# Kernel tuning notes

Measured on AMD Instinct MI355X. Metric: run time of the kernel, lower is better.

Reference implementation:

```python
import jax, jax.numpy as jnp
import numpy as np

C = 32          # in_channels = out_channels = groups
K = 3           # kernel_size
STRIDE = 2
PAD = 1
DIL = 1
EPS = 1e-20


def _depthwise_convT(x, w):
    """Equivalent of torch.F.conv_transpose2d(x, w, groups=C, stride=STRIDE,
    padding=PAD, dilation=DIL) with w of shape (C, 1, K, K).
    Implemented as an lhs-dilated conv with a spatially flipped kernel."""
    w_f = w[:, :, ::-1, ::-1]
    pad = DIL * (K - 1) - PAD  # = 1 for K=3, PAD=1, DIL=1
    return jax.lax.conv_general_dilated(
        x, w_f,
        window_strides=(1, 1),
        padding=[(pad, pad), (pad, pad)],
        lhs_dilation=(STRIDE, STRIDE),
        rhs_dilation=(DIL, DIL),
        dimension_numbers=('NCHW', 'OIHW', 'NCHW'),
        feature_group_count=C)


def setup_inputs() -> dict:
    key = jax.random.key(0)
    k = jax.random.split(key, 7)
    B, H, W = 2, 176, 608
    # depths/confidences are positive (rand); gy is signed (randn)
    d = jax.random.uniform(k[0], (B, C, H, W), dtype=jnp.float32) + 0.5
    cd = jax.random.uniform(k[1], (B, C, H, W), dtype=jnp.float32)
    gy = jax.random.normal(k[2], (B, C, H, W), dtype=jnp.float32)
    cgy = jax.random.uniform(k[3], (B, C, H, W), dtype=jnp.float32)
    w_prop_raw = jax.random.normal(k[4], (1, C, 1, 1), dtype=jnp.float32)
    spatial_weight_raw = jax.random.normal(k[5], (C, 1, K, K), dtype=jnp.float32)
    bias = 0.01 * jax.random.normal(k[6], (1, C, 1, 1), dtype=jnp.float32)
    return {"d": d, "cd": cd, "gy": gy, "cgy": cgy,
            "w_prop_raw": w_prop_raw,
            "spatial_weight_raw": spatial_weight_raw,
            "bias": bias}


def reference(d, cd, gy, cgy, w_prop_raw, spatial_weight_raw, bias):
    # EnforcePos('softplus') on both learned weights
    w_prop = jax.nn.softplus(w_prop_raw)          # (1, C, 1, 1)
    sw = jax.nn.softplus(spatial_weight_raw)      # (C, 1, K, K)

    # roll-based vertical neighbor gather with edge confidence zeroing
    d_up = jnp.roll(d, 1, axis=2)
    cd_up = jnp.roll(cd, 1, axis=2).at[:, :, 0, :].set(0.0)
    d_down = jnp.roll(d, -1, axis=2)
    cd_down = jnp.roll(cd, -1, axis=2).at[:, :, -1, :].set(0.0)

    cgy_from_ds = cd_up * cd_up
    height = (cd_up * d_up + cd_down * d_down) / (cd_up + cd_down)
    gy_from_ds = (d_down - d_up) / 2.0 / height

    gy_f = (w_prop * cgy * gy + cgy_from_ds * gy_from_ds) / (w_prop * cgy + cgy_from_ds)
    cgy_f = (w_prop * cgy + cgy_from_ds) / (w_prop + 1.0)

    nom = _depthwise_convT(cgy_f * gy_f, sw)
    denom = _depthwise_convT(cgy_f, sw)
    cdenom = _depthwise_convT(jnp.ones_like(cgy_f), sw)

    # original adds bias twice: once unconditionally, once under use_bias
    gy_out = nom / (denom + EPS) + bias + bias
    cgy_out = denom / (cdenom + EPS)
    return gy_out / STRIDE, cgy_out
```

## Files before the change

kernel.cpp:

```cpp
#include <hip/hip_runtime.h>
#include <math.h>

#define B_   2
#define C_   32
#define H_   176
#define W_   608
#define HO_  351
#define WO_  1215
#define PLANE_O (HO_ * WO_)
#define OUT1_O  (B_ * C_ * PLANE_O)
#define EPS_ 1e-20f
#define NTH  512
#define W4   (W_ / 4)
#define HW_  304

typedef float f4_t __attribute__((ext_vector_type(4)));
typedef float f2_t __attribute__((ext_vector_type(2)));

__device__ __forceinline__ float softplus_f(float x) {
    return fmaxf(x, 0.0f) + log1pf(expf(-fabsf(x)));
}

extern "C" __global__ __launch_bounds__(NTH, 8)
void structn_rows(const float* __restrict__ d,
                  const float* __restrict__ cd,
                  const float* __restrict__ gy,
                  const float* __restrict__ cgy,
                  const float* __restrict__ wpr,
                  const float* __restrict__ swr,
                  const float* __restrict__ bias,
                  float* __restrict__ out)
{
    __shared__ float s_nE[5 * HW_];
    __shared__ float s_nO[5 * HW_];
    __shared__ float s_cE[5 * HW_];
    __shared__ float s_cO[5 * HW_];

    const int g     = blockIdx.x;
    const int plane = blockIdx.y;
    const int c     = plane & (C_ - 1);

    float sw[9];
#pragma unroll
    for (int k = 0; k < 9; ++k) sw[k] = softplus_f(swr[c * 9 + k]);
    const float wp      = softplus_f(wpr[c]);
    const float inv_wp1 = 1.0f / (wp + 1.0f);
    const float bv      = bias[c];
    const float icd_ee  = 1.0f / (sw[4] + EPS_);
    const float icd_eo  = 1.0f / (sw[3] + sw[5] + EPS_);
    const float icd_oe  = 1.0f / (sw[1] + sw[7] + EPS_);
    const float icd_oo  = 1.0f / (sw[0] + sw[2] + sw[6] + sw[8] + EPS_);

    const int r0  = g * 4;
    const int nrf = (r0 + 4 <= H_ - 1) ? 5 : (H_ - r0);

    const int pbase = plane * (H_ * W_);
    const float* __restrict__ dP  = d   + pbase;
    const float* __restrict__ cdP = cd  + pbase;
    const float* __restrict__ gyP = gy  + pbase;
    const float* __restrict__ cgP = cgy + pbase;

    const int ntask = nrf * W4;
    for (int idx = threadIdx.x; idx < ntask; idx += NTH) {
        const int rf = idx / W4;
        const int iw = (idx - rf * W4) << 2;
        const int iy = r0 + rf;
        const int up = (iy == 0)      ? (H_ - 1) : iy - 1;
        const int dn = (iy == H_ - 1) ? 0        : iy + 1;
        const float mu = (iy > 0)      ? 1.0f : 0.0f;
        const float md = (iy < H_ - 1) ? 1.0f : 0.0f;

        const f4_t du = *(const f4_t*)(dP  + up * W_ + iw);
        const f4_t dd = *(const f4_t*)(dP  + dn * W_ + iw);
        const f4_t cu = *(const f4_t*)(cdP + up * W_ + iw);
        const f4_t cn = *(const f4_t*)(cdP + dn * W_ + iw);
        const f4_t gg = *(const f4_t*)(gyP + iy * W_ + iw);
        const f4_t cg = *(const f4_t*)(cgP + iy * W_ + iw);

        f4_t sn4, sc4;
#pragma unroll
        for (int e = 0; e < 4; ++e) {
            const float cuv = cu[e] * mu;
            const float cnv = cn[e] * md;
            const float cfd = cuv * cuv;
            const float rs  = __builtin_amdgcn_rcpf(fmaf(cuv, du[e], cnv * dd[e]));
            const float gfd = 0.5f * (dd[e] - du[e]) * (cuv + cnv) * rs;
            const float num = fmaf(wp * cg[e], gg[e], cfd * gfd);
            const float den = fmaf(wp, cg[e], cfd);
            sn4[e] = num * inv_wp1;
            sc4[e] = den * inv_wp1;
        }
        const int eo = rf * HW_ + (iw >> 1);
        f2_t v;
        v[0] = sn4[0]; v[1] = sn4[2];  *(f2_t*)(s_nE + eo) = v;
        v[0] = sn4[1]; v[1] = sn4[3];  *(f2_t*)(s_nO + eo) = v;
        v[0] = sc4[0]; v[1] = sc4[2];  *(f2_t*)(s_cE + eo) = v;
        v[0] = sc4[1]; v[1] = sc4[3];  *(f2_t*)(s_cO + eo) = v;
    }
    __syncthreads();

    const int w    = threadIdx.x >> 6;
    const int lane = threadIdx.x & 63;
    const int oy   = g * 8 + w;
    if (oy >= HO_) return;

    const int p   = w & 1;
    const int lrA = w >> 1;

    const int ro0 = plane * PLANE_O + oy * WO_;
    float* __restrict__ o0 = out + ro0;
    float* __restrict__ o1 = out + OUT1_O + ro0;

    const int h  = (4 - (ro0 & 3)) & 3;
    const int n4 = (WO_ - h) >> 2;
    const int q  = h & 1;
    const int r  = (h >> 1) & 1;

    const float icdC = p ? icd_oe : icd_ee;
    const float icdO = p ? icd_oo : icd_eo;
    const float i0 = q ? icdO : icdC;
    const float i1 = q ? icdC : icdO;

    const float* __restrict__ nAE = s_nE + lrA * HW_;
    const float* __restrict__ nAO = s_nO + lrA * HW_;
    const float* __restrict__ cAE = s_cE + lrA * HW_;
    const float* __restrict__ cAO = s_cO + lrA * HW_;

#define VAL(E, O, j) (((j) & 1) ? (O)[((j) - 1) >> 1] : (E)[(j) >> 1])

    if (p == 0) {
        if (lane < 3) {
            const int ox = (lane < h) ? lane : (h + (n4 << 2) + lane - h);
            float den, nom, icd;
            if ((ox & 1) == 0) {
                const int j = ox >> 1;
                den = VAL(cAE, cAO, j) * sw[4];
                nom = VAL(nAE, nAO, j) * sw[4];
                icd = icd_ee;
            } else {
                const int j = (ox - 1) >> 1;
                den = VAL(cAE, cAO, j) * sw[5] + VAL(cAE, cAO, j + 1) * sw[3];
                nom = VAL(nAE, nAO, j) * sw[5] + VAL(nAE, nAO, j + 1) * sw[3];
                icd = icd_eo;
            }
            o0[ox] = fmaf(0.5f * nom, __builtin_amdgcn_rcpf(den + EPS_), bv);
            o1[ox] = den * icd;
        }
        const float* pa0 = r ? nAO : nAE;
        const float* pa1 = r ? nAE + 1 : nAO;
        const float* pa2 = r ? nAO + 1 : nAE + 1;
        const float* px0 = r ? cAO : cAE;
        const float* px1 = r ? cAE + 1 : cAO;
        const float* px2 = r ? cAO + 1 : cAE + 1;

        for (int k = lane; k < n4; k += 64) {
            const float a0 = pa0[k], a1 = pa1[k], a2 = pa2[k];
            const float x0 = px0[k], x1 = px1[k], x2 = px2[k];
            const float dC0 = x0 * sw[4], dC1 = x1 * sw[4], dC2 = x2 * sw[4];
            const float nC0 = a0 * sw[4], nC1 = a1 * sw[4], nC2 = a2 * sw[4];
            const float dF0 = x0 * sw[5] + x1 * sw[3];
            const float dF1 = x1 * sw[5] + x2 * sw[3];
            const float nF0 = a0 * sw[5] + a1 * sw[3];
            const float nF1 = a1 * sw[5] + a2 * sw[3];

            const float d0 = q ? dF0 : dC0, n0 = q ? nF0 : nC0;
            const float d1 = q ? dC1 : dF0, n1 = q ? nC1 : nF0;
            const float d2 = q ? dF1 : dC1, n2 = q ? nF1 : nC1;
            const float d3 = q ? dC2 : dF1, n3 = q ? nC2 : nF1;

            f4_t gv, qv;
            gv[0] = fmaf(0.5f * n0, __builtin_amdgcn_rcpf(d0 + EPS_), bv);
            gv[1] = fmaf(0.5f * n1, __builtin_amdgcn_rcpf(d1 + EPS_), bv);
            gv[2] = fmaf(0.5f * n2, __builtin_amdgcn_rcpf(d2 + EPS_), bv);
            gv[3] = fmaf(0.5f * n3, __builtin_amdgcn_rcpf(d3 + EPS_), bv);
            qv[0] = d0 * i0; qv[1] = d1 * i1; qv[2] = d2 * i0; qv[3] = d3 * i1;

            const int c0 = h + (k << 2);
            __builtin_nontemporal_store(gv, (f4_t*)(o0 + c0));
            __builtin_nontemporal_store(qv, (f4_t*)(o1 + c0));
        }
    } else {
        const float* __restrict__ nBE = nAE + HW_;
        const float* __restrict__ nBO = nAO + HW_;
        const float* __restrict__ cBE = cAE + HW_;
        const float* __restrict__ cBO = cAO + HW_;

        if (lane < 3) {
            const int ox = (lane < h) ? lane : (h + (n4 << 2) + lane - h);
            float den, nom, icd;
            if ((ox & 1) == 0) {
                const int j = ox >> 1;
                den = VAL(cAE, cAO, j) * sw[7] + VAL(cBE, cBO, j) * sw[1];
                nom = VAL(nAE, nAO, j) * sw[7] + VAL(nBE, nBO, j) * sw[1];
                icd = icd_oe;
            } else {
                const int j = (ox - 1) >> 1;
                den = VAL(cAE, cAO, j) * sw[8] + VAL(cAE, cAO, j + 1) * sw[6]
                    + VAL(cBE, cBO, j) * sw[2] + VAL(cBE, cBO, j + 1) * sw[0];
                nom = VAL(nAE, nAO, j) * sw[8] + VAL(nAE, nAO, j + 1) * sw[6]
                    + VAL(nBE, nBO, j) * sw[2] + VAL(nBE, nBO, j + 1) * sw[0];
                icd = icd_oo;
            }
            o0[ox] = fmaf(0.5f * nom, __builtin_amdgcn_rcpf(den + EPS_), bv);
            o1[ox] = den * icd;
        }

        const float* pa0 = r ? nAO : nAE;
        const float* pa1 = r ? nAE + 1 : nAO;
        const float* pa2 = r ? nAO + 1 : nAE + 1;
        const float* px0 = r ? cAO : cAE;
        const float* px1 = r ? cAE + 1 : cAO;
        const float* px2 = r ? cAO + 1 : cAE + 1;
        const float* pb0 = r ? nBO : nBE;
        const float* pb1 = r ? nBE + 1 : nBO;
        const float* pb2 = r ? nBO + 1 : nBE + 1;
        const float* py0 = r ? cBO : cBE;
        const float* py1 = r ? cBE + 1 : cBO;
        const float* py2 = r ? cBO + 1 : cBE + 1;

        for (int k = lane; k < n4; k += 64) {
            const float a0 = pa0[k], a1 = pa1[k], a2 = pa2[k];
            const float x0 = px0[k], x1 = px1[k], x2 = px2[k];
            const float b0 = pb0[k], b1 = pb1[k], b2 = pb2[k];
            const float y0 = py0[k], y1 = py1[k], y2 = py2[k];

            const float dC0 = x0 * sw[7] + y0 * sw[1];
            const float dC1 = x1 * sw[7] + y1 * sw[1];
            const float dC2 = x2 * sw[7] + y2 * sw[1];
            const float nC0 = a0 * sw[7] + b0 * sw[1];
            const float nC1 = a1 * sw[7] + b1 * sw[1];
            const float nC2 = a2 * sw[7] + b2 * sw[1];
            const float dF0 = x0 * sw[8] + x1 * sw[6] + y0 * sw[2] + y1 * sw[0];
            const float dF1 = x1 * sw[8] + x2 * sw[6] + y1 * sw[2] + y2 * sw[0];
            const float nF0 = a0 * sw[8] + a1 * sw[6] + b0 * sw[2] + b1 * sw[0];
            const float nF1 = a1 * sw[8] + a2 * sw[6] + b1 * sw[2] + b2 * sw[0];

            const float d0 = q ? dF0 : dC0, n0 = q ? nF0 : nC0;
            const float d1 = q ? dC1 : dF0, n1 = q ? nC1 : nF0;
            const float d2 = q ? dF1 : dC1, n2 = q ? nF1 : nC1;
            const float d3 = q ? dC2 : dF1, n3 = q ? nC2 : nF1;

            f4_t gv, qv;
            gv[0] = fmaf(0.5f * n0, __builtin_amdgcn_rcpf(d0 + EPS_), bv);
            gv[1] = fmaf(0.5f * n1, __builtin_amdgcn_rcpf(d1 + EPS_), bv);
            gv[2] = fmaf(0.5f * n2, __builtin_amdgcn_rcpf(d2 + EPS_), bv);
            gv[3] = fmaf(0.5f * n3, __builtin_amdgcn_rcpf(d3 + EPS_), bv);
            qv[0] = d0 * i0; qv[1] = d1 * i1; qv[2] = d2 * i0; qv[3] = d3 * i1;

            const int c0 = h + (k << 2);
            __builtin_nontemporal_store(gv, (f4_t*)(o0 + c0));
            __builtin_nontemporal_store(qv, (f4_t*)(o1 + c0));
        }
    }
#undef VAL
}

extern "C" void kernel_launch(void* const* d_in, const int* in_sizes, int n_in,
                              void* d_out, int out_size, void* d_ws, size_t ws_size,
                              hipStream_t stream) {
    const float* d    = (const float*)d_in[0];
    const float* cd   = (const float*)d_in[1];
    const float* gy   = (const float*)d_in[2];
    const float* cgy  = (const float*)d_in[3];
    const float* wpr  = (const float*)d_in[4];
    const float* swr  = (const float*)d_in[5];
    const float* bias = (const float*)d_in[6];
    float* out = (float*)d_out;

    dim3 grid(44, B_ * C_);
    structn_rows<<<grid, NTH, 0, stream>>>(d, cd, gy, cgy, wpr, swr, bias, out);
}
```

Measured before the change: 73.81 us.

## Halve block size and rows per block, hoist stage-1 loads, simplify pointer setup

```diff
diff --git a/kernel.cpp b/kernel.cpp
--- a/kernel.cpp
+++ b/kernel.cpp
@@ -10,9 +10,10 @@
 #define PLANE_O (HO_ * WO_)
 #define OUT1_O  (B_ * C_ * PLANE_O)
 #define EPS_ 1e-20f
-#define NTH  512
+#define NTH  256
 #define W4   (W_ / 4)
 #define HW_  304
+#define NROWS 3
 
 typedef float f4_t __attribute__((ext_vector_type(4)));
 typedef float f2_t __attribute__((ext_vector_type(2)));
@@ -31,10 +32,10 @@
                   const float* __restrict__ bias,
                   float* __restrict__ out)
 {
-    __shared__ float s_nE[5 * HW_];
-    __shared__ float s_nO[5 * HW_];
-    __shared__ float s_cE[5 * HW_];
-    __shared__ float s_cO[5 * HW_];
+    __shared__ float s_nE[NROWS * HW_];
+    __shared__ float s_nO[NROWS * HW_];
+    __shared__ float s_cE[NROWS * HW_];
+    __shared__ float s_cO[NROWS * HW_];
 
     const int g     = blockIdx.x;
     const int plane = blockIdx.y;
@@ -51,8 +52,8 @@
     const float icd_oe  = 1.0f / (sw[1] + sw[7] + EPS_);
     const float icd_oo  = 1.0f / (sw[0] + sw[2] + sw[6] + sw[8] + EPS_);
 
-    const int r0  = g * 4;
-    const int nrf = (r0 + 4 <= H_ - 1) ? 5 : (H_ - r0);
+    const int r0  = g * 2;
+    const int nrf = (r0 + NROWS - 1 <= H_ - 1) ? NROWS : (H_ - r0);
 
     const int pbase = plane * (H_ * W_);
     const float* __restrict__ dP  = d   + pbase;
@@ -61,47 +62,76 @@
     const float* __restrict__ cgP = cgy + pbase;
 
     const int ntask = nrf * W4;
-    for (int idx = threadIdx.x; idx < ntask; idx += NTH) {
-        const int rf = idx / W4;
-        const int iw = (idx - rf * W4) << 2;
-        const int iy = r0 + rf;
-        const int up = (iy == 0)      ? (H_ - 1) : iy - 1;
-        const int dn = (iy == H_ - 1) ? 0        : iy + 1;
-        const float mu = (iy > 0)      ? 1.0f : 0.0f;
-        const float md = (iy < H_ - 1) ? 1.0f : 0.0f;
-
-        const f4_t du = *(const f4_t*)(dP  + up * W_ + iw);
-        const f4_t dd = *(const f4_t*)(dP  + dn * W_ + iw);
-        const f4_t cu = *(const f4_t*)(cdP + up * W_ + iw);
-        const f4_t cn = *(const f4_t*)(cdP + dn * W_ + iw);
-        const f4_t gg = *(const f4_t*)(gyP + iy * W_ + iw);
-        const f4_t cg = *(const f4_t*)(cgP + iy * W_ + iw);
-
-        f4_t sn4, sc4;
-#pragma unroll
-        for (int e = 0; e < 4; ++e) {
-            const float cuv = cu[e] * mu;
-            const float cnv = cn[e] * md;
-            const float cfd = cuv * cuv;
-            const float rs  = __builtin_amdgcn_rcpf(fmaf(cuv, du[e], cnv * dd[e]));
-            const float gfd = 0.5f * (dd[e] - du[e]) * (cuv + cnv) * rs;
-            const float num = fmaf(wp * cg[e], gg[e], cfd * gfd);
-            const float den = fmaf(wp, cg[e], cfd);
-            sn4[e] = num * inv_wp1;
-            sc4[e] = den * inv_wp1;
-        }
-        const int eo = rf * HW_ + (iw >> 1);
-        f2_t v;
-        v[0] = sn4[0]; v[1] = sn4[2];  *(f2_t*)(s_nE + eo) = v;
-        v[0] = sn4[1]; v[1] = sn4[3];  *(f2_t*)(s_nO + eo) = v;
-        v[0] = sc4[0]; v[1] = sc4[2];  *(f2_t*)(s_cE + eo) = v;
-        v[0] = sc4[1]; v[1] = sc4[3];  *(f2_t*)(s_cO + eo) = v;
+    const int idx0  = threadIdx.x;
+    const int idx1  = threadIdx.x + NTH;
+    const bool has1 = (idx1 < ntask);
+
+    const int rfA = idx0 / W4;
+    const int iwA = (idx0 - rfA * W4) << 2;
+    const int iyA = r0 + rfA;
+    const int upA = (iyA == 0)      ? (H_ - 1) : iyA - 1;
+    const int dnA = (iyA == H_ - 1) ? 0        : iyA + 1;
+    const float muA = (iyA > 0)      ? 1.0f : 0.0f;
+    const float mdA = (iyA < H_ - 1) ? 1.0f : 0.0f;
+
+    const f4_t duA = *(const f4_t*)(dP  + upA * W_ + iwA);
+    const f4_t ddA = *(const f4_t*)(dP  + dnA * W_ + iwA);
+    const f4_t cuA = *(const f4_t*)(cdP + upA * W_ + iwA);
+    const f4_t cnA = *(const f4_t*)(cdP + dnA * W_ + iwA);
+    const f4_t ggA = *(const f4_t*)(gyP + iyA * W_ + iwA);
+    const f4_t cgA = *(const f4_t*)(cgP + iyA * W_ + iwA);
+
+    f4_t duB, ddB, cuB, cnB, ggB, cgB;
+    int rfB = 0, iwB = 0;
+    float muB = 0.f, mdB = 0.f;
+    if (has1) {
+        rfB = idx1 / W4;
+        iwB = (idx1 - rfB * W4) << 2;
+        const int iyB = r0 + rfB;
+        const int upB = (iyB == 0)      ? (H_ - 1) : iyB - 1;
+        const int dnB = (iyB == H_ - 1) ? 0        : iyB + 1;
+        muB = (iyB > 0)      ? 1.0f : 0.0f;
+        mdB = (iyB < H_ - 1) ? 1.0f : 0.0f;
+        duB = *(const f4_t*)(dP  + upB * W_ + iwB);
+        ddB = *(const f4_t*)(dP  + dnB * W_ + iwB);
+        cuB = *(const f4_t*)(cdP + upB * W_ + iwB);
+        cnB = *(const f4_t*)(cdP + dnB * W_ + iwB);
+        ggB = *(const f4_t*)(gyP + iyB * W_ + iwB);
+        cgB = *(const f4_t*)(cgP + iyB * W_ + iwB);
     }
+
+#define FUSE_STORE(du, dd, cu, cn, gg, cg, mu, md, rf, iw)                      \
+    {                                                                           \
+        f4_t sn4, sc4;                                                          \
+        _Pragma("unroll")                                                       \
+        for (int e = 0; e < 4; ++e) {                                           \
+            const float cuv = (cu)[e] * (mu);                                   \
+            const float cnv = (cn)[e] * (md);                                   \
+            const float cfd = cuv * cuv;                                        \
+            const float rs  = __builtin_amdgcn_rcpf(fmaf(cuv, (du)[e], cnv * (dd)[e])); \
+            const float gfd = 0.5f * ((dd)[e] - (du)[e]) * (cuv + cnv) * rs;    \
+            const float num = fmaf(wp * (cg)[e], (gg)[e], cfd * gfd);           \
+            const float den = fmaf(wp, (cg)[e], cfd);                           \
+            sn4[e] = num * inv_wp1;                                             \
+            sc4[e] = den * inv_wp1;                                             \
+        }                                                                       \
+        const int eo = (rf) * HW_ + ((iw) >> 1);                                \
+        f2_t v;                                                                 \
+        v[0] = sn4[0]; v[1] = sn4[2];  *(f2_t*)(s_nE + eo) = v;                 \
+        v[0] = sn4[1]; v[1] = sn4[3];  *(f2_t*)(s_nO + eo) = v;                 \
+        v[0] = sc4[0]; v[1] = sc4[2];  *(f2_t*)(s_cE + eo) = v;                 \
+        v[0] = sc4[1]; v[1] = sc4[3];  *(f2_t*)(s_cO + eo) = v;                 \
+    }
+
+    FUSE_STORE(duA, ddA, cuA, cnA, ggA, cgA, muA, mdA, rfA, iwA)
+    if (has1) FUSE_STORE(duB, ddB, cuB, cnB, ggB, cgB, muB, mdB, rfB, iwB)
+#undef FUSE_STORE
+
     __syncthreads();
 
     const int w    = threadIdx.x >> 6;
     const int lane = threadIdx.x & 63;
-    const int oy   = g * 8 + w;
+    const int oy   = g * 4 + w;
     if (oy >= HO_) return;
 
     const int p   = w & 1;
@@ -148,14 +178,12 @@
         }
         const float* pa0 = r ? nAO : nAE;
         const float* pa1 = r ? nAE + 1 : nAO;
-        const float* pa2 = r ? nAO + 1 : nAE + 1;
         const float* px0 = r ? cAO : cAE;
         const float* px1 = r ? cAE + 1 : cAO;
-        const float* px2 = r ? cAO + 1 : cAE + 1;
 
         for (int k = lane; k < n4; k += 64) {
-            const float a0 = pa0[k], a1 = pa1[k], a2 = pa2[k];
-            const float x0 = px0[k], x1 = px1[k], x2 = px2[k];
+            const float a0 = pa0[k], a1 = pa1[k], a2 = pa0[k + 1];
+            const float x0 = px0[k], x1 = px1[k], x2 = px0[k + 1];
             const float dC0 = x0 * sw[4], dC1 = x1 * sw[4], dC2 = x2 * sw[4];
             const float nC0 = a0 * sw[4], nC1 = a1 * sw[4], nC2 = a2 * sw[4];
             const float dF0 = x0 * sw[5] + x1 * sw[3];
@@ -207,22 +235,18 @@
 
         const float* pa0 = r ? nAO : nAE;
         const float* pa1 = r ? nAE + 1 : nAO;
-        const float* pa2 = r ? nAO + 1 : nAE + 1;
         const float* px0 = r ? cAO : cAE;
         const float* px1 = r ? cAE + 1 : cAO;
-        const float* px2 = r ? cAO + 1 : cAE + 1;
         const float* pb0 = r ? nBO : nBE;
         const float* pb1 = r ? nBE + 1 : nBO;
-        const float* pb2 = r ? nBO + 1 : nBE + 1;
         const float* py0 = r ? cBO : cBE;
         const float* py1 = r ? cBE + 1 : cBO;
-        const float* py2 = r ? cBO + 1 : cBE + 1;
 
         for (int k = lane; k < n4; k += 64) {
-            const float a0 = pa0[k], a1 = pa1[k], a2 = pa2[k];
-            const float x0 = px0[k], x1 = px1[k], x2 = px2[k];
-            const float b0 = pb0[k], b1 = pb1[k], b2 = pb2[k];
-            const float y0 = py0[k], y1 = py1[k], y2 = py2[k];
+            const float a0 = pa0[k], a1 = pa1[k], a2 = pa0[k + 1];
+            const float x0 = px0[k], x1 = px1[k], x2 = px0[k + 1];
+            const float b0 = pb0[k], b1 = pb1[k], b2 = pb0[k + 1];
+            const float y0 = py0[k], y1 = py1[k], y2 = py0[k + 1];
 
             const float dC0 = x0 * sw[7] + y0 * sw[1];
             const float dC1 = x1 * sw[7] + y1 * sw[1];
@@ -267,6 +291,6 @@
     const float* bias = (const float*)d_in[6];
     float* out = (float*)d_out;
 
-    dim3 grid(44, B_ * C_);
+    dim3 grid(88, B_ * C_);
     structn_rows<<<grid, NTH, 0, stream>>>(d, cd, gy, cgy, wpr, swr, bias, out);
 }
```

New measurement: 86.87 us. 1.18x slower.

## Recompute fused input stage per output row instead of staging in shared memory

Applied to the files above, without the earlier changes.

```diff
diff --git a/kernel.cpp b/kernel.cpp
--- a/kernel.cpp
+++ b/kernel.cpp
@@ -11,31 +11,68 @@
 #define OUT1_O  (B_ * C_ * PLANE_O)
 #define EPS_ 1e-20f
 #define NTH  512
-#define W4   (W_ / 4)
-#define HW_  304
 
 typedef float f4_t __attribute__((ext_vector_type(4)));
-typedef float f2_t __attribute__((ext_vector_type(2)));
 
 __device__ __forceinline__ float softplus_f(float x) {
     return fmaxf(x, 0.0f) + log1pf(expf(-fabsf(x)));
 }
 
-extern "C" __global__ __launch_bounds__(NTH, 8)
-void structn_rows(const float* __restrict__ d,
-                  const float* __restrict__ cd,
-                  const float* __restrict__ gy,
-                  const float* __restrict__ cgy,
-                  const float* __restrict__ wpr,
-                  const float* __restrict__ swr,
-                  const float* __restrict__ bias,
-                  float* __restrict__ out)
+__device__ __forceinline__ void fused1(const float* __restrict__ dP,
+                                       const float* __restrict__ cdP,
+                                       const float* __restrict__ gyP,
+                                       const float* __restrict__ cgP,
+                                       int i, int j, float wp, float inv_wp1,
+                                       float& n, float& c)
 {
-    __shared__ float s_nE[5 * HW_];
-    __shared__ float s_nO[5 * HW_];
-    __shared__ float s_cE[5 * HW_];
-    __shared__ float s_cO[5 * HW_];
-
+    const int up = (i == 0)      ? (H_ - 1) : i - 1;
+    const int dn = (i == H_ - 1) ? 0        : i + 1;
+    const float mu = (i > 0)      ? 1.0f : 0.0f;
+    const float md = (i < H_ - 1) ? 1.0f : 0.0f;
+    const float du = dP[up * W_ + j];
+    const float dd = dP[dn * W_ + j];
+    const float cu = cdP[up * W_ + j] * mu;
+    const float cn = cdP[dn * W_ + j] * md;
+    const float g  = gyP[i * W_ + j];
+    const float cg = cgP[i * W_ + j];
+    const float cfd = cu * cu;
+    const float rs  = __builtin_amdgcn_rcpf(fmaf(cu, du, cn * dd));
+    const float gfd = 0.5f * (dd - du) * (cu + cn) * rs;
+    n = fmaf(wp * cg, g, cfd * gfd) * inv_wp1;
+    c = fmaf(wp, cg, cfd) * inv_wp1;
+}
+
+__device__ __forceinline__ void fused3(const f4_t du, const f4_t dd,
+                                       const f4_t cu_, const f4_t cn_,
+                                       const f4_t gg, const f4_t cg,
+                                       float mu, float md,
+                                       float wp, float inv_wp1,
+                                       float n[3], float c[3])
+{
+#pragma unroll
+    for (int e = 0; e < 3; ++e) {
+        const float cuv = cu_[e] * mu;
+        const float cnv = cn_[e] * md;
+        const float cfd = cuv * cuv;
+        const float rs  = __builtin_amdgcn_rcpf(fmaf(cuv, du[e], cnv * dd[e]));
+        const float gfd = 0.5f * (dd[e] - du[e]) * (cuv + cnv) * rs;
+        n[e] = fmaf(wp * cg[e], gg[e], cfd * gfd) * inv_wp1;
+        c[e] = fmaf(wp, cg[e], cfd) * inv_wp1;
+    }
+}
+
+#define LD4(p) (*(const f4_t*)(p))
+
+extern "C" __global__ __launch_bounds__(NTH)
+void structn_direct(const float* __restrict__ d,
+                    const float* __restrict__ cd,
+                    const float* __restrict__ gy,
+                    const float* __restrict__ cgy,
+                    const float* __restrict__ wpr,
+                    const float* __restrict__ swr,
+                    const float* __restrict__ bias,
+                    float* __restrict__ out)
+{
     const int g     = blockIdx.x;
     const int plane = blockIdx.y;
     const int c     = plane & (C_ - 1);
@@ -51,117 +88,94 @@
     const float icd_oe  = 1.0f / (sw[1] + sw[7] + EPS_);
     const float icd_oo  = 1.0f / (sw[0] + sw[2] + sw[6] + sw[8] + EPS_);
 
-    const int r0  = g * 4;
-    const int nrf = (r0 + 4 <= H_ - 1) ? 5 : (H_ - r0);
-
     const int pbase = plane * (H_ * W_);
     const float* __restrict__ dP  = d   + pbase;
     const float* __restrict__ cdP = cd  + pbase;
     const float* __restrict__ gyP = gy  + pbase;
     const float* __restrict__ cgP = cgy + pbase;
 
-    const int ntask = nrf * W4;
-    for (int idx = threadIdx.x; idx < ntask; idx += NTH) {
-        const int rf = idx / W4;
-        const int iw = (idx - rf * W4) << 2;
-        const int iy = r0 + rf;
-        const int up = (iy == 0)      ? (H_ - 1) : iy - 1;
-        const int dn = (iy == H_ - 1) ? 0        : iy + 1;
-        const float mu = (iy > 0)      ? 1.0f : 0.0f;
-        const float md = (iy < H_ - 1) ? 1.0f : 0.0f;
-
-        const f4_t du = *(const f4_t*)(dP  + up * W_ + iw);
-        const f4_t dd = *(const f4_t*)(dP  + dn * W_ + iw);
-        const f4_t cu = *(const f4_t*)(cdP + up * W_ + iw);
-        const f4_t cn = *(const f4_t*)(cdP + dn * W_ + iw);
-        const f4_t gg = *(const f4_t*)(gyP + iy * W_ + iw);
-        const f4_t cg = *(const f4_t*)(cgP + iy * W_ + iw);
-
-        f4_t sn4, sc4;
-#pragma unroll
-        for (int e = 0; e < 4; ++e) {
-            const float cuv = cu[e] * mu;
-            const float cnv = cn[e] * md;
-            const float cfd = cuv * cuv;
-            const float rs  = __builtin_amdgcn_rcpf(fmaf(cuv, du[e], cnv * dd[e]));
-            const float gfd = 0.5f * (dd[e] - du[e]) * (cuv + cnv) * rs;
-            const float num = fmaf(wp * cg[e], gg[e], cfd * gfd);
-            const float den = fmaf(wp, cg[e], cfd);
-            sn4[e] = num * inv_wp1;
-            sc4[e] = den * inv_wp1;
-        }
-        const int eo = rf * HW_ + (iw >> 1);
-        f2_t v;
-        v[0] = sn4[0]; v[1] = sn4[2];  *(f2_t*)(s_nE + eo) = v;
-        v[0] = sn4[1]; v[1] = sn4[3];  *(f2_t*)(s_nO + eo) = v;
-        v[0] = sc4[0]; v[1] = sc4[2];  *(f2_t*)(s_cE + eo) = v;
-        v[0] = sc4[1]; v[1] = sc4[3];  *(f2_t*)(s_cO + eo) = v;
-    }
-    __syncthreads();
-
     const int w    = threadIdx.x >> 6;
     const int lane = threadIdx.x & 63;
     const int oy   = g * 8 + w;
     if (oy >= HO_) return;
 
-    const int p   = w & 1;
-    const int lrA = w >> 1;
+    const int p = oy & 1;
+    const int i = oy >> 1;
 
     const int ro0 = plane * PLANE_O + oy * WO_;
     float* __restrict__ o0 = out + ro0;
     float* __restrict__ o1 = out + OUT1_O + ro0;
 
     const int h  = (4 - (ro0 & 3)) & 3;
-    const int n4 = (WO_ - h) >> 2;
+    const int jb = h >> 1;
     const int q  = h & 1;
-    const int r  = (h >> 1) & 1;
 
     const float icdC = p ? icd_oe : icd_ee;
     const float icdO = p ? icd_oo : icd_eo;
     const float i0 = q ? icdO : icdC;
     const float i1 = q ? icdC : icdO;
 
-    const float* __restrict__ nAE = s_nE + lrA * HW_;
-    const float* __restrict__ nAO = s_nO + lrA * HW_;
-    const float* __restrict__ cAE = s_cE + lrA * HW_;
-    const float* __restrict__ cAO = s_cO + lrA * HW_;
-
-#define VAL(E, O, j) (((j) & 1) ? (O)[((j) - 1) >> 1] : (E)[(j) >> 1])
+    if (lane < 7) {
+        const int ox = (lane < h) ? lane : 1208 + lane;
+        float den, nom;
+        if ((ox & 1) == 0) {
+            const int j = ox >> 1;
+            float nA, cA;
+            fused1(dP, cdP, gyP, cgP, i, j, wp, inv_wp1, nA, cA);
+            if (p == 0) { den = cA * sw[4]; nom = nA * sw[4]; }
+            else {
+                float nB, cB;
+                fused1(dP, cdP, gyP, cgP, i + 1, j, wp, inv_wp1, nB, cB);
+                den = cA * sw[7] + cB * sw[1];
+                nom = nA * sw[7] + nB * sw[1];
+            }
+        } else {
+            const int j = (ox - 1) >> 1;
+            float nA0, cA0, nA1, cA1;
+            fused1(dP, cdP, gyP, cgP, i, j,     wp, inv_wp1, nA0, cA0);
+            fused1(dP, cdP, gyP, cgP, i, j + 1, wp, inv_wp1, nA1, cA1);
+            if (p == 0) {
+                den = cA0 * sw[5] + cA1 * sw[3];
+                nom = nA0 * sw[5] + nA1 * sw[3];
+            } else {
+                float nB0, cB0, nB1, cB1;
+                fused1(dP, cdP, gyP, cgP, i + 1, j,     wp, inv_wp1, nB0, cB0);
+                fused1(dP, cdP, gyP, cgP, i + 1, j + 1, wp, inv_wp1, nB1, cB1);
+                den = cA0 * sw[8] + cA1 * sw[6] + cB0 * sw[2] + cB1 * sw[0];
+                nom = nA0 * sw[8] + nA1 * sw[6] + nB0 * sw[2] + nB1 * sw[0];
+            }
+        }
+        const float icd = (ox & 1) ? icdO : icdC;
+        o0[ox] = fmaf(0.5f * nom, __builtin_amdgcn_rcpf(den + EPS_), bv);
+        o1[ox] = den * icd;
+    }
+
+    const int upA = (i == 0)      ? (H_ - 1) : i - 1;
+    const int dnA = (i == H_ - 1) ? 0        : i + 1;
+    const float muA = (i > 0)      ? 1.0f : 0.0f;
+    const float mdA = (i < H_ - 1) ? 1.0f : 0.0f;
+    const float* __restrict__ dUA  = dP  + upA * W_;
+    const float* __restrict__ dDA  = dP  + dnA * W_;
+    const float* __restrict__ cUA  = cdP + upA * W_;
+    const float* __restrict__ cDA  = cdP + dnA * W_;
+    const float* __restrict__ gA   = gyP + i * W_;
+    const float* __restrict__ cgA  = cgP + i * W_;
 
     if (p == 0) {
-        if (lane < 3) {
-            const int ox = (lane < h) ? lane : (h + (n4 << 2) + lane - h);
-            float den, nom, icd;
-            if ((ox & 1) == 0) {
-                const int j = ox >> 1;
-                den = VAL(cAE, cAO, j) * sw[4];
-                nom = VAL(nAE, nAO, j) * sw[4];
-                icd = icd_ee;
-            } else {
-                const int j = (ox - 1) >> 1;
-                den = VAL(cAE, cAO, j) * sw[5] + VAL(cAE, cAO, j + 1) * sw[3];
-                nom = VAL(nAE, nAO, j) * sw[5] + VAL(nAE, nAO, j + 1) * sw[3];
-                icd = icd_eo;
-            }
-            o0[ox] = fmaf(0.5f * nom, __builtin_amdgcn_rcpf(den + EPS_), bv);
-            o1[ox] = den * icd;
-        }
-        const float* pa0 = r ? nAO : nAE;
-        const float* pa1 = r ? nAE + 1 : nAO;
-        const float* pa2 = r ? nAO + 1 : nAE + 1;
-        const float* px0 = r ? cAO : cAE;
-        const float* px1 = r ? cAE + 1 : cAO;
-        const float* px2 = r ? cAO + 1 : cAE + 1;
-
-        for (int k = lane; k < n4; k += 64) {
-            const float a0 = pa0[k], a1 = pa1[k], a2 = pa2[k];
-            const float x0 = px0[k], x1 = px1[k], x2 = px2[k];
-            const float dC0 = x0 * sw[4], dC1 = x1 * sw[4], dC2 = x2 * sw[4];
-            const float nC0 = a0 * sw[4], nC1 = a1 * sw[4], nC2 = a2 * sw[4];
-            const float dF0 = x0 * sw[5] + x1 * sw[3];
-            const float dF1 = x1 * sw[5] + x2 * sw[3];
-            const float nF0 = a0 * sw[5] + a1 * sw[3];
-            const float nF1 = a1 * sw[5] + a2 * sw[3];
+        for (int k = lane; k < 302; k += 64) {
+            const int j0 = jb + 2 * k;
+            const f4_t du = LD4(dUA + j0), dd = LD4(dDA + j0);
+            const f4_t cu = LD4(cUA + j0), cn = LD4(cDA + j0);
+            const f4_t gg = LD4(gA  + j0), cg = LD4(cgA + j0);
+            float nA[3], cA[3];
+            fused3(du, dd, cu, cn, gg, cg, muA, mdA, wp, inv_wp1, nA, cA);
+
+            const float dC0 = cA[0] * sw[4], dC1 = cA[1] * sw[4], dC2 = cA[2] * sw[4];
+            const float nC0 = nA[0] * sw[4], nC1 = nA[1] * sw[4], nC2 = nA[2] * sw[4];
+            const float dF0 = cA[0] * sw[5] + cA[1] * sw[3];
+            const float dF1 = cA[1] * sw[5] + cA[2] * sw[3];
+            const float nF0 = nA[0] * sw[5] + nA[1] * sw[3];
+            const float nF1 = nA[1] * sw[5] + nA[2] * sw[3];
 
             const float d0 = q ? dF0 : dC0, n0 = q ? nF0 : nC0;
             const float d1 = q ? dC1 : dF0, n1 = q ? nC1 : nF0;
@@ -180,60 +194,39 @@
             __builtin_nontemporal_store(qv, (f4_t*)(o1 + c0));
         }
     } else {
-        const float* __restrict__ nBE = nAE + HW_;
-        const float* __restrict__ nBO = nAO + HW_;
-        const float* __restrict__ cBE = cAE + HW_;
-        const float* __restrict__ cBO = cAO + HW_;
-
-        if (lane < 3) {
-            const int ox = (lane < h) ? lane : (h + (n4 << 2) + lane - h);
-            float den, nom, icd;
-            if ((ox & 1) == 0) {
-                const int j = ox >> 1;
-                den = VAL(cAE, cAO, j) * sw[7] + VAL(cBE, cBO, j) * sw[1];
-                nom = VAL(nAE, nAO, j) * sw[7] + VAL(nBE, nBO, j) * sw[1];
-                icd = icd_oe;
-            } else {
-                const int j = (ox - 1) >> 1;
-                den = VAL(cAE, cAO, j) * sw[8] + VAL(cAE, cAO, j + 1) * sw[6]
-                    + VAL(cBE, cBO, j) * sw[2] + VAL(cBE, cBO, j + 1) * sw[0];
-                nom = VAL(nAE, nAO, j) * sw[8] + VAL(nAE, nAO, j + 1) * sw[6]
-                    + VAL(nBE, nBO, j) * sw[2] + VAL(nBE, nBO, j + 1) * sw[0];
-                icd = icd_oo;
-            }
-            o0[ox] = fmaf(0.5f * nom, __builtin_amdgcn_rcpf(den + EPS_), bv);
-            o1[ox] = den * icd;
-        }
-
-        const float* pa0 = r ? nAO : nAE;
-        const float* pa1 = r ? nAE + 1 : nAO;
-        const float* pa2 = r ? nAO + 1 : nAE + 1;
-        const float* px0 = r ? cAO : cAE;
-        const float* px1 = r ? cAE + 1 : cAO;
-        const float* px2 = r ? cAO + 1 : cAE + 1;
-        const float* pb0 = r ? nBO : nBE;
-        const float* pb1 = r ? nBE + 1 : nBO;
-        const float* pb2 = r ? nBO + 1 : nBE + 1;
-        const float* py0 = r ? cBO : cBE;
-        const float* py1 = r ? cBE + 1 : cBO;
-        const float* py2 = r ? cBO + 1 : cBE + 1;
-
-        for (int k = lane; k < n4; k += 64) {
-            const float a0 = pa0[k], a1 = pa1[k], a2 = pa2[k];
-            const float x0 = px0[k], x1 = px1[k], x2 = px2[k];
-            const float b0 = pb0[k], b1 = pb1[k], b2 = pb2[k];
-            const float y0 = py0[k], y1 = py1[k], y2 = py2[k];
-
-            const float dC0 = x0 * sw[7] + y0 * sw[1];
-            const float dC1 = x1 * sw[7] + y1 * sw[1];
-            const float dC2 = x2 * sw[7] + y2 * sw[1];
-            const float nC0 = a0 * sw[7] + b0 * sw[1];
-            const float nC1 = a1 * sw[7] + b1 * sw[1];
-            const float nC2 = a2 * sw[7] + b2 * sw[1];
-            const float dF0 = x0 * sw[8] + x1 * sw[6] + y0 * sw[2] + y1 * sw[0];
-            const float dF1 = x1 * sw[8] + x2 * sw[6] + y1 * sw[2] + y2 * sw[0];
-            const float nF0 = a0 * sw[8] + a1 * sw[6] + b0 * sw[2] + b1 * sw[0];
-            const float nF1 = a1 * sw[8] + a2 * sw[6] + b1 * sw[2] + b2 * sw[0];
+        const int iB  = i + 1;
+        const int dnB = (iB == H_ - 1) ? 0 : iB + 1;
+        const float mdB = (iB < H_ - 1) ? 1.0f : 0.0f;
+        const float* __restrict__ dUB  = dP  + i * W_;
+        const float* __restrict__ dDB  = dP  + dnB * W_;
+        const float* __restrict__ cUB  = cdP + i * W_;
+        const float* __restrict__ cDB  = cdP + dnB * W_;
+        const float* __restrict__ gB   = gyP + iB * W_;
+        const float* __restrict__ cgB  = cgP + iB * W_;
+
+        for (int k = lane; k < 302; k += 64) {
+            const int j0 = jb + 2 * k;
+            const f4_t duA4 = LD4(dUA + j0), ddA4 = LD4(dDA + j0);
+            const f4_t cuA4 = LD4(cUA + j0), cnA4 = LD4(cDA + j0);
+            const f4_t ggA4 = LD4(gA  + j0), cgA4 = LD4(cgA + j0);
+            const f4_t duB4 = LD4(dUB + j0), ddB4 = LD4(dDB + j0);
+            const f4_t cuB4 = LD4(cUB + j0), cnB4 = LD4(cDB + j0);
+            const f4_t ggB4 = LD4(gB  + j0), cgB4 = LD4(cgB + j0);
+
+            float nA[3], cA[3], nB[3], cB[3];
+            fused3(duA4, ddA4, cuA4, cnA4, ggA4, cgA4, muA, mdA, wp, inv_wp1, nA, cA);
+            fused3(duB4, ddB4, cuB4, cnB4, ggB4, cgB4, 1.0f, mdB, wp, inv_wp1, nB, cB);
+
+            const float dC0 = cA[0] * sw[7] + cB[0] * sw[1];
+            const float dC1 = cA[1] * sw[7] + cB[1] * sw[1];
+            const float dC2 = cA[2] * sw[7] + cB[2] * sw[1];
+            const float nC0 = nA[0] * sw[7] + nB[0] * sw[1];
+            const float nC1 = nA[1] * sw[7] + nB[1] * sw[1];
+            const float nC2 = nA[2] * sw[7] + nB[2] * sw[1];
+            const float dF0 = cA[0] * sw[8] + cA[1] * sw[6] + cB[0] * sw[2] + cB[1] * sw[0];
+            const float dF1 = cA[1] * sw[8] + cA[2] * sw[6] + cB[1] * sw[2] + cB[2] * sw[0];
+            const float nF0 = nA[0] * sw[8] + nA[1] * sw[6] + nB[0] * sw[2] + nB[1] * sw[0];
+            const float nF1 = nA[1] * sw[8] + nA[2] * sw[6] + nB[1] * sw[2] + nB[2] * sw[0];
 
             const float d0 = q ? dF0 : dC0, n0 = q ? nF0 : nC0;
             const float d1 = q ? dC1 : dF0, n1 = q ? nC1 : nF0;
@@ -252,7 +245,6 @@
             __builtin_nontemporal_store(qv, (f4_t*)(o1 + c0));
         }
     }
-#undef VAL
 }
 
 extern "C" void kernel_launch(void* const* d_in, const int* in_sizes, int n_in,
@@ -268,5 +260,5 @@
     float* out = (float*)d_out;
 
     dim3 grid(44, B_ * C_);
-    structn_rows<<<grid, NTH, 0, stream>>>(d, cd, gy, cgy, wpr, swr, bias, out);
-}
+    structn_direct<<<grid, NTH, 0, stream>>>(d, cd, gy, cgy, wpr, swr, bias, out);
+}
```

Result: slower. 88.75 us (+20.2%).
